# Kernel optimization log

Hardware: AMD Instinct MI355X
Metric: run time of the kernel (lower is better)

## Reference

```python
import jax, jax.numpy as jnp
import numpy as np

H = 4096  # hidden_size
B, S = 4, 2048
LN_EPS = 1e-5


def setup_inputs() -> dict:
    key = jax.random.key(0)
    ks = jax.random.split(key, 8)
    return {
        "x": jax.random.normal(ks[0], (B, S, H), dtype=jnp.float32),
        "ln_gamma": jnp.ones((H,), dtype=jnp.float32),
        "ln_beta": jnp.zeros((H,), dtype=jnp.float32),
        "w_mu": jax.random.normal(ks[1], (H, H), dtype=jnp.float32) * 0.02,
        "w_rho": jax.random.normal(ks[2], (H, H), dtype=jnp.float32) * 0.1,  # posterior_rho_init=0.0, std 0.1
        "b_mu": jax.random.normal(ks[3], (H,), dtype=jnp.float32) * 0.02,
        "b_rho": jax.random.normal(ks[4], (H,), dtype=jnp.float32) * 0.1,
        "eps_w": jax.random.normal(ks[5], (H, H), dtype=jnp.float32),
        "eps_b": jax.random.normal(ks[6], (H,), dtype=jnp.float32),
    }


def reference(x, ln_gamma, ln_beta, w_mu, w_rho, b_mu, b_rho, eps_w, eps_b):
    residual = x
    # LayerNorm over last dim
    mean = jnp.mean(x, axis=-1, keepdims=True)
    var = jnp.var(x, axis=-1, keepdims=True)
    h = (x - mean) * jax.lax.rsqrt(var + LN_EPS) * ln_gamma + ln_beta
    # Bayesian reparameterized linear: W = mu + softplus(rho) * eps
    W = w_mu + jax.nn.softplus(w_rho) * eps_w            # [H_out, H_in]
    b = b_mu + jax.nn.softplus(b_rho) * eps_b            # [H_out]
    y = jnp.einsum("bsh,oh->bso", h, W) + b
    # exact (erf) GELU, matching torch.nn.functional.gelu default
    y = jax.nn.gelu(y, approximate=False)
    return residual + y
```

## Files before the change

### kernel.cpp

```cpp
#include <hip/hip_runtime.h>
#include <hip/hip_bf16.h>
#include <cstdint>
#include <cstddef>

#define HDIM 4096
#define MROWS 8192
#define LN_EPS 1e-5f

typedef __bf16 bf16_t;
typedef __bf16 bf16x4_t __attribute__((ext_vector_type(4)));
typedef __bf16 bf16x8_t __attribute__((ext_vector_type(8)));
typedef float f32x4_t __attribute__((ext_vector_type(4)));

typedef const __attribute__((address_space(1))) void gvoid_t;
typedef __attribute__((address_space(3))) void lvoid_t;

__device__ __forceinline__ float softplus_f(float x) {
    return fmaxf(x, 0.f) + log1pf(expf(-fabsf(x)));
}

__global__ __launch_bounds__(256) void wgen_kernel(
    const float* __restrict__ mu, const float* __restrict__ rho,
    const float* __restrict__ eps, bf16_t* __restrict__ W)
{
    int i = (blockIdx.x * 256 + threadIdx.x) * 4;
    float4 m = *(const float4*)(mu + i);
    float4 r = *(const float4*)(rho + i);
    float4 e = *(const float4*)(eps + i);
    bf16x4_t o;
    o[0] = (bf16_t)(m.x + softplus_f(r.x) * e.x);
    o[1] = (bf16_t)(m.y + softplus_f(r.y) * e.y);
    o[2] = (bf16_t)(m.z + softplus_f(r.z) * e.z);
    o[3] = (bf16_t)(m.w + softplus_f(r.w) * e.w);
    *(bf16x4_t*)(W + i) = o;
}

__global__ __launch_bounds__(256) void biasgen_kernel(
    const float* __restrict__ mu, const float* __restrict__ rho,
    const float* __restrict__ eps, float* __restrict__ b)
{
    int i = blockIdx.x * 256 + threadIdx.x;
    b[i] = mu[i] + softplus_f(rho[i]) * eps[i];
}

__global__ __launch_bounds__(256) void ln_kernel(
    const float* __restrict__ x, const float* __restrict__ gamma,
    const float* __restrict__ beta, bf16_t* __restrict__ h)
{
    int row = blockIdx.x;
    const float* xr = x + (size_t)row * HDIM;
    int t = threadIdx.x;
    float4 v[4];
    float s = 0.f, s2 = 0.f;
#pragma unroll
    for (int j = 0; j < 4; ++j) {
        v[j] = *(const float4*)(xr + j * 1024 + t * 4);
        s  += v[j].x + v[j].y + v[j].z + v[j].w;
        s2 += v[j].x * v[j].x + v[j].y * v[j].y + v[j].z * v[j].z + v[j].w * v[j].w;
    }
#pragma unroll
    for (int off = 32; off > 0; off >>= 1) {
        s  += __shfl_down(s, off);
        s2 += __shfl_down(s2, off);
    }
    __shared__ float ps[4], ps2[4];
    if ((t & 63) == 0) { ps[t >> 6] = s; ps2[t >> 6] = s2; }
    __syncthreads();
    float tot  = ps[0] + ps[1] + ps[2] + ps[3];
    float tot2 = ps2[0] + ps2[1] + ps2[2] + ps2[3];
    float mean = tot * (1.f / HDIM);
    float var  = tot2 * (1.f / HDIM) - mean * mean;
    float rstd = rsqrtf(var + LN_EPS);
    bf16_t* hr = h + (size_t)row * HDIM;
#pragma unroll
    for (int j = 0; j < 4; ++j) {
        int c = j * 1024 + t * 4;
        float4 g  = *(const float4*)(gamma + c);
        float4 bb = *(const float4*)(beta + c);
        bf16x4_t o;
        o[0] = (bf16_t)((v[j].x - mean) * rstd * g.x + bb.x);
        o[1] = (bf16_t)((v[j].y - mean) * rstd * g.y + bb.y);
        o[2] = (bf16_t)((v[j].z - mean) * rstd * g.z + bb.z);
        o[3] = (bf16_t)((v[j].w - mean) * rstd * g.w + bb.w);
        *(bf16x4_t*)(hr + c) = o;
    }
}

__device__ __forceinline__ void gload_lds16(const bf16_t* g, const char* l) {
    __builtin_amdgcn_global_load_lds((gvoid_t*)g, (lvoid_t*)l, 16, 0, 0);
}

__device__ __forceinline__ bf16x8_t ds_read_b128_raw(const char* p) {
    f32x4_t r;
    asm volatile("ds_read_b128 %0, %1" : "=v"(r) : "v"((lvoid_t*)p));
    return __builtin_bit_cast(bf16x8_t, r);
}

__device__ __forceinline__ int swz(int x) { return x ^ ((x >> 3) & 0x30); }

__global__ __launch_bounds__(512, 2) void gemm_kernel(
    const bf16_t* __restrict__ A,
    const bf16_t* __restrict__ B,
    const float* __restrict__ bias,
    const float* __restrict__ xres,
    float* __restrict__ out)
{
    __shared__ char lds[131072];

    const int tid  = threadIdx.x;
    const int lane = tid & 63, w = tid >> 6;
    const int g = lane >> 4, fr = lane & 15;
    const int wm = w >> 2, wn = w & 3;

    int bid = blockIdx.x;
    int wg  = (bid & 7) * 64 + (bid >> 3);
    const int tileN = (wg & 15) * 256;
    const int tileM = (wg >> 4) * 256;

    const bf16_t* srcA[2];
    const bf16_t* srcB[2];
    int ldstA[2], ldstB[2];
#pragma unroll
    for (int r = 0; r < 2; ++r) {
        int D = r * 8192 + w * 1024 + lane * 16;
        int S = swz(D);
        int row = S >> 6, colel = (S & 63) >> 1;
        srcA[r] = A + (size_t)(tileM + row) * HDIM + colel;
        srcB[r] = B + (size_t)(tileN + row) * HDIM + colel;
        ldstA[r] = r * 8192 + w * 1024;
        ldstB[r] = 16384 + r * 8192 + w * 1024;
    }

    int aoff[8], boff[4];
#pragma unroll
    for (int m = 0; m < 8; ++m)
        aoff[m] = swz(wm * 8192 + m * 1024 + fr * 64 + g * 16);
#pragma unroll
    for (int n = 0; n < 4; ++n)
        boff[n] = 16384 + swz(wn * 4096 + n * 1024 + fr * 64 + g * 16);

    f32x4_t acc[8][4] = {};
    const int NT = HDIM / 32;

    bf16x8_t af0, af1, af2, af3, af4, af5, af6, af7;
    bf16x8_t bv0, bv1, bv2, bv3;

#define STAGE_A(bb, kofs)                                        \
    do {                                                         \
        gload_lds16(srcA[0] + (kofs), &lds[(bb) + ldstA[0]]);    \
        gload_lds16(srcA[1] + (kofs), &lds[(bb) + ldstA[1]]);    \
    } while (0)
#define STAGE_B(bb, kofs)                                        \
    do {                                                         \
        gload_lds16(srcB[0] + (kofs), &lds[(bb) + ldstB[0]]);    \
        gload_lds16(srcB[1] + (kofs), &lds[(bb) + ldstB[1]]);    \
    } while (0)
#define CL(AF, R)                                                               \
    acc[R][0] = __builtin_amdgcn_mfma_f32_16x16x32_bf16(AF, bv0, acc[R][0], 0, 0, 0); \
    acc[R][1] = __builtin_amdgcn_mfma_f32_16x16x32_bf16(AF, bv1, acc[R][1], 0, 0, 0); \
    acc[R][2] = __builtin_amdgcn_mfma_f32_16x16x32_bf16(AF, bv2, acc[R][2], 0, 0, 0); \
    acc[R][3] = __builtin_amdgcn_mfma_f32_16x16x32_bf16(AF, bv3, acc[R][3], 0, 0, 0);
#define SCHEDB __builtin_amdgcn_sched_barrier(0)
#define BARRIER do { __builtin_amdgcn_s_barrier(); SCHEDB; } while (0)
#define LGKM0 do { asm volatile("s_waitcnt lgkmcnt(0)" ::: "memory"); SCHEDB; } while (0)
#define VMCNT8 do { asm volatile("s_waitcnt vmcnt(8)" ::: "memory"); SCHEDB; } while (0)

    STAGE_A(0, 0);      STAGE_B(0, 0);
    STAGE_A(32768, 32); STAGE_B(32768, 32);
    STAGE_A(65536, 64); STAGE_B(65536, 64);
    asm volatile("s_waitcnt vmcnt(8)" ::: "memory");
    BARRIER;

#pragma unroll 1
    for (int t = 0; t < NT; ++t) {
        const char* buf = &lds[(t & 3) * 32768];
        const int sb = ((t + 3) & 3) * 32768;
        const int sk = ((t + 3) & (NT - 1)) * 32;

        af0 = ds_read_b128_raw(buf + aoff[0]);
        af1 = ds_read_b128_raw(buf + aoff[1]);
        af2 = ds_read_b128_raw(buf + aoff[2]);
        af3 = ds_read_b128_raw(buf + aoff[3]);
        bv0 = ds_read_b128_raw(buf + boff[0]);
        bv1 = ds_read_b128_raw(buf + boff[1]);
        bv2 = ds_read_b128_raw(buf + boff[2]);
        bv3 = ds_read_b128_raw(buf + boff[3]);
        STAGE_A(sb, sk);
        SCHEDB;
        LGKM0;
        __builtin_amdgcn_s_setprio(1);
        CL(af0, 0) CL(af1, 1) CL(af2, 2) CL(af3, 3)
        __builtin_amdgcn_s_setprio(0);
        SCHEDB;
        BARRIER;

        af4 = ds_read_b128_raw(buf + aoff[4]);
        af5 = ds_read_b128_raw(buf + aoff[5]);
        af6 = ds_read_b128_raw(buf + aoff[6]);
        af7 = ds_read_b128_raw(buf + aoff[7]);
        STAGE_B(sb, sk);
        SCHEDB;
        LGKM0;
        __builtin_amdgcn_s_setprio(1);
        CL(af4, 4) CL(af5, 5) CL(af6, 6) CL(af7, 7)
        __builtin_amdgcn_s_setprio(0);
        SCHEDB;
        VMCNT8;
        BARRIER;
    }
#undef STAGE_A
#undef STAGE_B

    const int col0 = tileN + wn * 64 + fr;
    const int row0 = tileM + wm * 128 + g * 4;
#pragma unroll
    for (int n = 0; n < 4; ++n) {
        float bvv = bias[col0 + n * 16];
#pragma unroll
        for (int m = 0; m < 8; ++m) {
#pragma unroll
            for (int j = 0; j < 4; ++j) {
                size_t idx = (size_t)(row0 + m * 16 + j) * HDIM + (col0 + n * 16);
                float v = acc[m][n][j] + bvv;
                float ge = 0.5f * v * (1.0f + erff(v * 0.70710678118654752f));
                out[idx] = xres[idx] + ge;
            }
        }
    }
}

extern "C" void kernel_launch(void* const* d_in, const int* in_sizes, int n_in,
                              void* d_out, int out_size, void* d_ws, size_t ws_size,
                              hipStream_t stream) {
    const float* x        = (const float*)d_in[0];
    const float* ln_gamma = (const float*)d_in[1];
    const float* ln_beta  = (const float*)d_in[2];
    const float* w_mu     = (const float*)d_in[3];
    const float* w_rho    = (const float*)d_in[4];
    const float* b_mu     = (const float*)d_in[5];
    const float* b_rho    = (const float*)d_in[6];
    const float* eps_w    = (const float*)d_in[7];
    const float* eps_b    = (const float*)d_in[8];
    float* out = (float*)d_out;

    char* ws = (char*)d_ws;
    bf16_t* h_bf16 = (bf16_t*)ws;
    bf16_t* W_bf16 = (bf16_t*)(ws + 67108864);
    float*  bias   = (float*)(ws + 67108864 + 33554432);

    wgen_kernel<<<16384, 256, 0, stream>>>(w_mu, w_rho, eps_w, W_bf16);
    biasgen_kernel<<<16, 256, 0, stream>>>(b_mu, b_rho, eps_b, bias);
    ln_kernel<<<MROWS, 256, 0, stream>>>(x, ln_gamma, ln_beta, h_bf16);
    gemm_kernel<<<512, 512, 0, stream>>>(h_bf16, W_bf16, bias, x, out);
}
```

Measured before the change: 428.8 us.

## Software-pipeline LDS fragment reads across k-tiles with register double buffering

Restructures the GEMM main loop so the A and B fragments for the next k-tile are read from LDS while the second half of the current tile's MFMAs run. Two register sets alternate across a 2x unrolled loop, and partial lgkmcnt waits replace full drains. The mid-iteration barrier is dropped and the global-load wait is tightened to vmcnt(4). This is meant to hide LDS read latency behind MFMA work and cut barrier stalls, at the cost of more VGPRs for fragment buffers and tighter reasoning about buffer reuse.

```diff
diff --git a/kernel.cpp b/kernel.cpp
--- a/kernel.cpp
+++ b/kernel.cpp
@@ -142,8 +142,9 @@
     f32x4_t acc[8][4] = {};
     const int NT = HDIM / 32;
 
-    bf16x8_t af0, af1, af2, af3, af4, af5, af6, af7;
-    bf16x8_t bv0, bv1, bv2, bv3;
+    bf16x8_t pa0, pa1, pa2, pa3, pv0, pv1, pv2, pv3;
+    bf16x8_t qa0, qa1, qa2, qa3;
+    bf16x8_t ra0, ra1, ra2, ra3, rv0, rv1, rv2, rv3;
 
 #define STAGE_A(bb, kofs)                                        \
     do {                                                         \
@@ -155,59 +156,75 @@
         gload_lds16(srcB[0] + (kofs), &lds[(bb) + ldstB[0]]);    \
         gload_lds16(srcB[1] + (kofs), &lds[(bb) + ldstB[1]]);    \
     } while (0)
-#define CL(AF, R)                                                               \
-    acc[R][0] = __builtin_amdgcn_mfma_f32_16x16x32_bf16(AF, bv0, acc[R][0], 0, 0, 0); \
-    acc[R][1] = __builtin_amdgcn_mfma_f32_16x16x32_bf16(AF, bv1, acc[R][1], 0, 0, 0); \
-    acc[R][2] = __builtin_amdgcn_mfma_f32_16x16x32_bf16(AF, bv2, acc[R][2], 0, 0, 0); \
-    acc[R][3] = __builtin_amdgcn_mfma_f32_16x16x32_bf16(AF, bv3, acc[R][3], 0, 0, 0);
+#define CL(AF, V, R)                                                            \
+    acc[R][0] = __builtin_amdgcn_mfma_f32_16x16x32_bf16(AF, V##0, acc[R][0], 0, 0, 0); \
+    acc[R][1] = __builtin_amdgcn_mfma_f32_16x16x32_bf16(AF, V##1, acc[R][1], 0, 0, 0); \
+    acc[R][2] = __builtin_amdgcn_mfma_f32_16x16x32_bf16(AF, V##2, acc[R][2], 0, 0, 0); \
+    acc[R][3] = __builtin_amdgcn_mfma_f32_16x16x32_bf16(AF, V##3, acc[R][3], 0, 0, 0);
 #define SCHEDB __builtin_amdgcn_sched_barrier(0)
-#define BARRIER do { __builtin_amdgcn_s_barrier(); SCHEDB; } while (0)
-#define LGKM0 do { asm volatile("s_waitcnt lgkmcnt(0)" ::: "memory"); SCHEDB; } while (0)
-#define VMCNT8 do { asm volatile("s_waitcnt vmcnt(8)" ::: "memory"); SCHEDB; } while (0)
+#define LGKM(n) do { asm volatile("s_waitcnt lgkmcnt(" #n ")" ::: "memory"); SCHEDB; } while (0)
+
+#define RDQ(tc)                                                       \
+    do { const char* bp_ = &lds[((tc) & 3) * 32768];                  \
+        qa0 = ds_read_b128_raw(bp_ + aoff[4]);                        \
+        qa1 = ds_read_b128_raw(bp_ + aoff[5]);                        \
+        qa2 = ds_read_b128_raw(bp_ + aoff[6]);                        \
+        qa3 = ds_read_b128_raw(bp_ + aoff[7]); } while (0)
+#define RDN(tc, SA, SV)                                               \
+    do { const char* bp_ = &lds[((tc) & 3) * 32768];                  \
+        SA##0 = ds_read_b128_raw(bp_ + aoff[0]);                      \
+        SA##1 = ds_read_b128_raw(bp_ + aoff[1]);                      \
+        SA##2 = ds_read_b128_raw(bp_ + aoff[2]);                      \
+        SA##3 = ds_read_b128_raw(bp_ + aoff[3]);                      \
+        SV##0 = ds_read_b128_raw(bp_ + boff[0]);                      \
+        SV##1 = ds_read_b128_raw(bp_ + boff[1]);                      \
+        SV##2 = ds_read_b128_raw(bp_ + boff[2]);                      \
+        SV##3 = ds_read_b128_raw(bp_ + boff[3]); } while (0)
+
+#define KTILE(tc, CA, CV, NA, NV)                                     \
+    do {                                                              \
+        const int sb_ = (((tc) + 3) & 3) * 32768;                     \
+        const int sk_ = (((tc) + 3) & (NT - 1)) * 32;                 \
+                                                         \
+        RDQ(tc);                                                      \
+        STAGE_A(sb_, sk_);                                            \
+        SCHEDB;                                                       \
+        LGKM(4);                                                      \
+        __builtin_amdgcn_s_setprio(1);                                \
+        CL(CA##0, CV, 0) CL(CA##1, CV, 1) CL(CA##2, CV, 2) CL(CA##3, CV, 3) \
+        __builtin_amdgcn_s_setprio(0);                                \
+        SCHEDB;                                                       \
+                                                         \
+        RDN((tc) + 1, NA, NV);                                        \
+        STAGE_B(sb_, sk_);                                            \
+        SCHEDB;                                                       \
+        LGKM(8);                                                      \
+        __builtin_amdgcn_s_setprio(1);                                \
+        CL(qa0, CV, 4) CL(qa1, CV, 5) CL(qa2, CV, 6) CL(qa3, CV, 7)   \
+        __builtin_amdgcn_s_setprio(0);                                \
+        SCHEDB;                                                       \
+        asm volatile("s_waitcnt vmcnt(4)" ::: "memory");              \
+        __builtin_amdgcn_s_barrier();                                 \
+        SCHEDB;                                                       \
+    } while (0)
 
     STAGE_A(0, 0);      STAGE_B(0, 0);
     STAGE_A(32768, 32); STAGE_B(32768, 32);
     STAGE_A(65536, 64); STAGE_B(65536, 64);
-    asm volatile("s_waitcnt vmcnt(8)" ::: "memory");
-    BARRIER;
+    asm volatile("s_waitcnt vmcnt(4)" ::: "memory");
+    __builtin_amdgcn_s_barrier();
+    SCHEDB;
+    RDN(0, pa, pv);
+    SCHEDB;
 
 #pragma unroll 1
-    for (int t = 0; t < NT; ++t) {
-        const char* buf = &lds[(t & 3) * 32768];
-        const int sb = ((t + 3) & 3) * 32768;
-        const int sk = ((t + 3) & (NT - 1)) * 32;
-
-        af0 = ds_read_b128_raw(buf + aoff[0]);
-        af1 = ds_read_b128_raw(buf + aoff[1]);
-        af2 = ds_read_b128_raw(buf + aoff[2]);
-        af3 = ds_read_b128_raw(buf + aoff[3]);
-        bv0 = ds_read_b128_raw(buf + boff[0]);
-        bv1 = ds_read_b128_raw(buf + boff[1]);
-        bv2 = ds_read_b128_raw(buf + boff[2]);
-        bv3 = ds_read_b128_raw(buf + boff[3]);
-        STAGE_A(sb, sk);
-        SCHEDB;
-        LGKM0;
-        __builtin_amdgcn_s_setprio(1);
-        CL(af0, 0) CL(af1, 1) CL(af2, 2) CL(af3, 3)
-        __builtin_amdgcn_s_setprio(0);
-        SCHEDB;
-        BARRIER;
-
-        af4 = ds_read_b128_raw(buf + aoff[4]);
-        af5 = ds_read_b128_raw(buf + aoff[5]);
-        af6 = ds_read_b128_raw(buf + aoff[6]);
-        af7 = ds_read_b128_raw(buf + aoff[7]);
-        STAGE_B(sb, sk);
-        SCHEDB;
-        LGKM0;
-        __builtin_amdgcn_s_setprio(1);
-        CL(af4, 4) CL(af5, 5) CL(af6, 6) CL(af7, 7)
-        __builtin_amdgcn_s_setprio(0);
-        SCHEDB;
-        VMCNT8;
-        BARRIER;
-    }
+    for (int t = 0; t < NT; t += 2) {
+        KTILE(t,     pa, pv, ra, rv);
+        KTILE(t + 1, ra, rv, pa, pv);
+    }
+#undef KTILE
+#undef RDQ
+#undef RDN
 #undef STAGE_A
 #undef STAGE_B
 
```

Result: faster. 419.3 us, median of 2 (-2.2%).

## Restructure GEMM mainloop to double-buffered BK=64 tiles with four-phase staging

Applied to the files above, without the earlier changes.

The GEMM main loop changes from a 4-deep ring of BK=32 LDS buffers to two 64 KB buffers holding BK=64 tiles. Each iteration now runs four MFMA phases, and the global-to-LDS loads for the next tile are spread across those phases. The LDS layout and XOR swizzle are redone for 128-byte rows. The aim is fewer loop iterations and barriers per K element and better spreading of load issue, at the cost of a shallower prefetch depth and more barriers per iteration.

```diff
diff --git a/kernel.cpp b/kernel.cpp
--- a/kernel.cpp
+++ b/kernel.cpp
@@ -96,8 +96,6 @@
     return __builtin_bit_cast(bf16x8_t, r);
 }
 
-__device__ __forceinline__ int swz(int x) { return x ^ ((x >> 3) & 0x30); }
-
 __global__ __launch_bounds__(512, 2) void gemm_kernel(
     const bf16_t* __restrict__ A,
     const bf16_t* __restrict__ B,
@@ -117,44 +115,28 @@
     const int tileN = (wg & 15) * 256;
     const int tileM = (wg >> 4) * 256;
 
-    const bf16_t* srcA[2];
-    const bf16_t* srcB[2];
-    int ldstA[2], ldstB[2];
-#pragma unroll
-    for (int r = 0; r < 2; ++r) {
-        int D = r * 8192 + w * 1024 + lane * 16;
-        int S = swz(D);
-        int row = S >> 6, colel = (S & 63) >> 1;
-        srcA[r] = A + (size_t)(tileM + row) * HDIM + colel;
-        srcB[r] = B + (size_t)(tileN + row) * HDIM + colel;
-        ldstA[r] = r * 8192 + w * 1024;
-        ldstB[r] = 16384 + r * 8192 + w * 1024;
-    }
+    const int srow = w * 8 + (lane >> 3);
+    const int scol = 8 * ((lane & 7) ^ (lane >> 3));
+    const bf16_t* srcA = A + (size_t)(tileM + srow) * HDIM + scol;
+    const bf16_t* srcB = B + (size_t)(tileN + srow) * HDIM + scol;
 
     int aoff[8], boff[4];
 #pragma unroll
-    for (int m = 0; m < 8; ++m)
-        aoff[m] = swz(wm * 8192 + m * 1024 + fr * 64 + g * 16);
-#pragma unroll
-    for (int n = 0; n < 4; ++n)
-        boff[n] = 16384 + swz(wn * 4096 + n * 1024 + fr * 64 + g * 16);
+    for (int m = 0; m < 8; ++m) {
+        int L = (wm * 128 + m * 16 + fr) * 128 + g * 16;
+        aoff[m] = L ^ (((L >> 7) & 7) << 4);
+    }
+#pragma unroll
+    for (int n = 0; n < 4; ++n) {
+        int L = (wn * 64 + n * 16 + fr) * 128 + g * 16;
+        boff[n] = 32768 + (L ^ (((L >> 7) & 7) << 4));
+    }
 
     f32x4_t acc[8][4] = {};
-    const int NT = HDIM / 32;
-
-    bf16x8_t af0, af1, af2, af3, af4, af5, af6, af7;
-    bf16x8_t bv0, bv1, bv2, bv3;
-
-#define STAGE_A(bb, kofs)                                        \
-    do {                                                         \
-        gload_lds16(srcA[0] + (kofs), &lds[(bb) + ldstA[0]]);    \
-        gload_lds16(srcA[1] + (kofs), &lds[(bb) + ldstA[1]]);    \
-    } while (0)
-#define STAGE_B(bb, kofs)                                        \
-    do {                                                         \
-        gload_lds16(srcB[0] + (kofs), &lds[(bb) + ldstB[0]]);    \
-        gload_lds16(srcB[1] + (kofs), &lds[(bb) + ldstB[1]]);    \
-    } while (0)
+    const int NT = HDIM / 64;
+
+    bf16x8_t af0, af1, af2, af3, bv0, bv1, bv2, bv3;
+
 #define CL(AF, R)                                                               \
     acc[R][0] = __builtin_amdgcn_mfma_f32_16x16x32_bf16(AF, bv0, acc[R][0], 0, 0, 0); \
     acc[R][1] = __builtin_amdgcn_mfma_f32_16x16x32_bf16(AF, bv1, acc[R][1], 0, 0, 0); \
@@ -163,19 +145,32 @@
 #define SCHEDB __builtin_amdgcn_sched_barrier(0)
 #define BARRIER do { __builtin_amdgcn_s_barrier(); SCHEDB; } while (0)
 #define LGKM0 do { asm volatile("s_waitcnt lgkmcnt(0)" ::: "memory"); SCHEDB; } while (0)
-#define VMCNT8 do { asm volatile("s_waitcnt vmcnt(8)" ::: "memory"); SCHEDB; } while (0)
-
-    STAGE_A(0, 0);      STAGE_B(0, 0);
-    STAGE_A(32768, 32); STAGE_B(32768, 32);
-    STAGE_A(65536, 64); STAGE_B(65536, 64);
-    asm volatile("s_waitcnt vmcnt(8)" ::: "memory");
-    BARRIER;
+#define VMCNT(n) do { asm volatile("s_waitcnt vmcnt(" #n ")" ::: "memory"); SCHEDB; } while (0)
+#define MFMA_BLK(A0, A1, A2, A3, R0, R1, R2, R3)       \
+    __builtin_amdgcn_s_setprio(1);                      \
+    CL(A0, R0) CL(A1, R1) CL(A2, R2) CL(A3, R3)         \
+    __builtin_amdgcn_s_setprio(0);                      \
+    SCHEDB;
+
+    {
+        char* s0 = &lds[0];
+        gload_lds16(srcB,              s0 + 32768 + w * 1024);
+        gload_lds16(srcB +  64 * HDIM, s0 + 32768 +  8192 + w * 1024);
+        gload_lds16(srcB + 128 * HDIM, s0 + 32768 + 16384 + w * 1024);
+        gload_lds16(srcB + 192 * HDIM, s0 + 32768 + 24576 + w * 1024);
+        gload_lds16(srcA,              s0 + w * 1024);
+        gload_lds16(srcA + 128 * HDIM, s0 + 16384 + w * 1024);
+        gload_lds16(srcA +  64 * HDIM, s0 +  8192 + w * 1024);
+        gload_lds16(srcA + 192 * HDIM, s0 + 24576 + w * 1024);
+        asm volatile("s_waitcnt vmcnt(0)" ::: "memory");
+        BARRIER;
+    }
 
 #pragma unroll 1
-    for (int t = 0; t < NT; ++t) {
-        const char* buf = &lds[(t & 3) * 32768];
-        const int sb = ((t + 3) & 3) * 32768;
-        const int sk = ((t + 3) & (NT - 1)) * 32;
+    for (int kt = 0; kt < NT; ++kt) {
+        const char* buf = &lds[(kt & 1) * 65536];
+        char* stg = &lds[((kt + 1) & 1) * 65536];
+        const int sk = ((kt + 1) & (NT - 1)) * 64;
 
         af0 = ds_read_b128_raw(buf + aoff[0]);
         af1 = ds_read_b128_raw(buf + aoff[1]);
@@ -185,31 +180,58 @@
         bv1 = ds_read_b128_raw(buf + boff[1]);
         bv2 = ds_read_b128_raw(buf + boff[2]);
         bv3 = ds_read_b128_raw(buf + boff[3]);
-        STAGE_A(sb, sk);
-        SCHEDB;
-        LGKM0;
-        __builtin_amdgcn_s_setprio(1);
-        CL(af0, 0) CL(af1, 1) CL(af2, 2) CL(af3, 3)
-        __builtin_amdgcn_s_setprio(0);
-        SCHEDB;
-        BARRIER;
-
-        af4 = ds_read_b128_raw(buf + aoff[4]);
-        af5 = ds_read_b128_raw(buf + aoff[5]);
-        af6 = ds_read_b128_raw(buf + aoff[6]);
-        af7 = ds_read_b128_raw(buf + aoff[7]);
-        STAGE_B(sb, sk);
-        SCHEDB;
-        LGKM0;
-        __builtin_amdgcn_s_setprio(1);
-        CL(af4, 4) CL(af5, 5) CL(af6, 6) CL(af7, 7)
-        __builtin_amdgcn_s_setprio(0);
-        SCHEDB;
-        VMCNT8;
-        BARRIER;
-    }
-#undef STAGE_A
-#undef STAGE_B
+        gload_lds16(srcB + sk,             stg + 32768 + w * 1024);
+        gload_lds16(srcB + 64 * HDIM + sk, stg + 32768 + 8192 + w * 1024);
+        SCHEDB;
+        VMCNT(2);
+        BARRIER;
+        LGKM0;
+        MFMA_BLK(af0, af1, af2, af3, 0, 1, 2, 3)
+        BARRIER;
+
+        af0 = ds_read_b128_raw(buf + aoff[4]);
+        af1 = ds_read_b128_raw(buf + aoff[5]);
+        af2 = ds_read_b128_raw(buf + aoff[6]);
+        af3 = ds_read_b128_raw(buf + aoff[7]);
+        gload_lds16(srcB + 128 * HDIM + sk, stg + 32768 + 16384 + w * 1024);
+        gload_lds16(srcB + 192 * HDIM + sk, stg + 32768 + 24576 + w * 1024);
+        SCHEDB;
+        BARRIER;
+        LGKM0;
+        MFMA_BLK(af0, af1, af2, af3, 4, 5, 6, 7)
+        BARRIER;
+
+        af0 = ds_read_b128_raw(buf + (aoff[0] ^ 64));
+        af1 = ds_read_b128_raw(buf + (aoff[1] ^ 64));
+        af2 = ds_read_b128_raw(buf + (aoff[2] ^ 64));
+        af3 = ds_read_b128_raw(buf + (aoff[3] ^ 64));
+        bv0 = ds_read_b128_raw(buf + (boff[0] ^ 64));
+        bv1 = ds_read_b128_raw(buf + (boff[1] ^ 64));
+        bv2 = ds_read_b128_raw(buf + (boff[2] ^ 64));
+        bv3 = ds_read_b128_raw(buf + (boff[3] ^ 64));
+        gload_lds16(srcA + sk,              stg + w * 1024);
+        gload_lds16(srcA + 128 * HDIM + sk, stg + 16384 + w * 1024);
+        SCHEDB;
+        BARRIER;
+        LGKM0;
+        MFMA_BLK(af0, af1, af2, af3, 0, 1, 2, 3)
+        BARRIER;
+
+        af0 = ds_read_b128_raw(buf + (aoff[4] ^ 64));
+        af1 = ds_read_b128_raw(buf + (aoff[5] ^ 64));
+        af2 = ds_read_b128_raw(buf + (aoff[6] ^ 64));
+        af3 = ds_read_b128_raw(buf + (aoff[7] ^ 64));
+        gload_lds16(srcA + 64 * HDIM + sk,  stg + 8192 + w * 1024);
+        gload_lds16(srcA + 192 * HDIM + sk, stg + 24576 + w * 1024);
+        SCHEDB;
+        VMCNT(2);
+        BARRIER;
+        LGKM0;
+        MFMA_BLK(af0, af1, af2, af3, 4, 5, 6, 7)
+        BARRIER;
+    }
+#undef MFMA_BLK
+#undef CL
 
     const int col0 = tileN + wn * 64 + fr;
     const int row0 = tileM + wm * 128 + g * 4;
```

New measurement: 437.1 us. Within noise of the previous version (+2.0%).
